# Optimization experiments

Hardware: AMD Instinct MI355X
Metric: run time of the kernel (lower is better)

The kernel has to match this reference:

```python
import jax, jax.numpy as jnp
import numpy as np

N = 100000
E = 1600000
IN_C, HID, OUT_C = 512, 256, 32
K = 10
ALPHA = 0.1


def setup_inputs() -> dict:
    key = jax.random.key(0)
    ks = jax.random.split(key, 8)
    x = jax.random.normal(ks[0], (N, IN_C), dtype=jnp.float32)
    edge_index = jax.random.randint(ks[1], (2, E), 0, N, dtype=jnp.int64)
    def lin(k, fan_in, fan_out):
        kw, kb = jax.random.split(k)
        bound = 1.0 / np.sqrt(fan_in)
        W = jax.random.uniform(kw, (fan_out, fan_in), minval=-bound, maxval=bound, dtype=jnp.float32)
        b = jax.random.uniform(kb, (fan_out,), minval=-bound, maxval=bound, dtype=jnp.float32)
        return W, b
    W1, b1 = lin(ks[2], IN_C, HID)
    Wr, br = lin(ks[3], HID, HID)
    W2, b2 = lin(ks[4], HID, OUT_C)
    return {"x": x, "edge_index": edge_index, "W1": W1, "b1": b1,
            "Wr": Wr, "br": br, "W2": W2, "b2": b2}


def _appnp(h0, row, col, norm):
    # h = (1-alpha) * A_hat h + alpha * h0, K steps
    def step(h, _):
        msg = norm[:, None] * h[row]                      # [E+N, C] gather
        agg = jax.ops.segment_sum(msg, col, num_segments=N)
        return (1.0 - ALPHA) * agg + ALPHA * h0, None
    h, _ = jax.lax.scan(step, h0, None, length=K)
    return h


def reference(x, edge_index, W1, b1, Wr, br, W2, b2):
    # eval mode: dropout p=0 -> identity
    h1 = jax.nn.relu(x @ W1.T + b1)
    h2 = jax.nn.relu(h1 @ Wr.T + br)
    x_res = h1 + h2
    h0 = x_res @ W2.T + b2                                # [N, OUT_C]

    # gcn_norm with self-loops (PyG default for APPNP)
    loops = jnp.arange(N, dtype=edge_index.dtype)
    row = jnp.concatenate([edge_index[0], loops])
    col = jnp.concatenate([edge_index[1], loops])
    deg = jax.ops.segment_sum(jnp.ones_like(col, dtype=h0.dtype), col, num_segments=N)
    dinv = jnp.where(deg > 0, jax.lax.rsqrt(deg), 0.0)
    norm = dinv[row] * dinv[col]                          # [E+N]

    return _appnp(h0, row, col, norm)
```

## Files before the change

### kernel.cpp

```cpp
#include <hip/hip_runtime.h>

#define N_NODES 100000
#define E_EDGES 1600000
#define IN_CH   512
#define HID     256
#define OUT_CH  32
#define K_STEPS 10
#define EPAD    (E_EDGES + 16 * N_NODES)

typedef unsigned short u16;
typedef unsigned int   u32;

typedef __attribute__((ext_vector_type(8))) short bf16x8;
typedef __attribute__((ext_vector_type(4))) float f32x4;

__device__ __forceinline__ float b2f(u16 u) {
    union { u32 i; float f; } x; x.i = ((u32)u) << 16; return x.f;
}
__device__ __forceinline__ u16 f2b(float f) {
    union { float f; u32 u; } x; x.f = f;
    u32 r = x.u + 0x7fffu + ((x.u >> 16) & 1u);
    return (u16)(r >> 16);
}

__device__ __forceinline__ void load_lds16(const void* g, void* l) {
    __builtin_amdgcn_global_load_lds(
        (const __attribute__((address_space(1))) unsigned int*)g,
        (__attribute__((address_space(3))) unsigned int*)l,
        16, 0, 0);
}


__global__ __launch_bounds__(256) void k_cast(const float* __restrict__ in, u16* __restrict__ out, int n4) {
    int i = blockIdx.x * 256 + threadIdx.x;
    if (i < n4) {
        float4 f = ((const float4*)in)[i];
        ushort4 u;
        u.x = f2b(f.x); u.y = f2b(f.y); u.z = f2b(f.z); u.w = f2b(f.w);
        ((ushort4*)out)[i] = u;
    }
}


__global__ __launch_bounds__(256) void k_count(const int* __restrict__ col, int* __restrict__ cnt) {
    int i = blockIdx.x * 256 + threadIdx.x;
    if (i < E_EDGES) atomicAdd(&cnt[col[i]], 1);
}

__global__ __launch_bounds__(256) void k_dinv(const int* __restrict__ cnt, float* __restrict__ dinv) {
    int i = blockIdx.x * 256 + threadIdx.x;
    if (i < N_NODES) dinv[i] = rsqrtf((float)(cnt[i] + 1));
}

__device__ __forceinline__ int pad16(int v) { return (v + 15) & ~15; }

__global__ __launch_bounds__(256) void k_blocksum(const int* __restrict__ cnt, int* __restrict__ bs) {
    int b = blockIdx.x, t = threadIdx.x;
    int idx = b * 1024 + t * 4;
    int s = 0;
    #pragma unroll
    for (int j = 0; j < 4; ++j) if (idx + j < N_NODES) s += pad16(cnt[idx + j]);
    #pragma unroll
    for (int d = 32; d > 0; d >>= 1) s += __shfl_down(s, d, 64);
    __shared__ int smem[4];
    int lane = t & 63, w = t >> 6;
    if (lane == 0) smem[w] = s;
    __syncthreads();
    if (t == 0) bs[b] = smem[0] + smem[1] + smem[2] + smem[3];
}

__global__ void k_scanblocks(const int* __restrict__ bs, int* __restrict__ bo, int nb) {
    int t = threadIdx.x;
    int v = (t < nb) ? bs[t] : 0;
    int incl = v;
    int lane = t & 63, w = t >> 6;
    #pragma unroll
    for (int d = 1; d < 64; d <<= 1) { int tt = __shfl_up(incl, d, 64); if (lane >= d) incl += tt; }
    __shared__ int wsum[2];
    if (lane == 63) wsum[w] = incl;
    __syncthreads();
    int add = (w == 1) ? wsum[0] : 0;
    if (t < nb) bo[t] = add + incl - v;
}

__global__ __launch_bounds__(256) void k_scanwithin(const int* __restrict__ cnt, const int* __restrict__ bo,
                                                    int* __restrict__ off) {
    int b = blockIdx.x, t = threadIdx.x;
    int idx = b * 1024 + t * 4;
    int v[4]; int s = 0;
    #pragma unroll
    for (int j = 0; j < 4; ++j) { v[j] = (idx + j < N_NODES) ? pad16(cnt[idx + j]) : 0; s += v[j]; }
    int incl = s;
    int lane = t & 63, w = t >> 6;
    #pragma unroll
    for (int d = 1; d < 64; d <<= 1) { int tt = __shfl_up(incl, d, 64); if (lane >= d) incl += tt; }
    __shared__ int wsum[4];
    if (lane == 63) wsum[w] = incl;
    __syncthreads();
    int woff = 0;
    #pragma unroll
    for (int k = 0; k < 4; ++k) if (k < w) woff += wsum[k];
    int run = bo[b] + woff + incl - s;
    #pragma unroll
    for (int j = 0; j < 4; ++j) { if (idx + j < N_NODES) off[idx + j] = run; run += v[j]; }
}

__global__ __launch_bounds__(256) void k_total(const int* __restrict__ bo, const int* __restrict__ bs,
                                               int* __restrict__ off, int nb) {
    off[N_NODES] = bo[nb - 1] + bs[nb - 1];
}

__global__ __launch_bounds__(256) void k_filldummy(int* __restrict__ csr_row) {
    int i = blockIdx.x * 256 + threadIdx.x;
    if (i < EPAD) csr_row[i] = N_NODES;
}

__global__ __launch_bounds__(256) void k_fill(const int* __restrict__ row, const int* __restrict__ col,
                                              const int* __restrict__ off, int* __restrict__ cursor,
                                              int* __restrict__ csr_row) {
    int i = blockIdx.x * 256 + threadIdx.x;
    if (i < E_EDGES) {
        int c = col[i];
        int pos = off[c] + atomicAdd(&cursor[c], 1);
        csr_row[pos] = row[i];
    }
}


__device__ __forceinline__ int swz_idx(int row, int col) {
    return row * 256 + (((col >> 3) ^ (row & 7)) << 3) + (col & 7);
}

__global__ __launch_bounds__(512, 2) void fused_mlp(const float* __restrict__ A,
                                                    const u16* __restrict__ W1b,
                                                    const float* __restrict__ b1,
                                                    const u16* __restrict__ Wrb,
                                                    const float* __restrict__ br,
                                                    const float* __restrict__ W2,
                                                    const float* __restrict__ b2,
                                                    const float* __restrict__ dinv,
                                                    float* __restrict__ h0,
                                                    u16* __restrict__ p0,
                                                    int M) {
    __shared__ __align__(16) u16 h1s[128 * 256];
    __shared__ __align__(16) u16 Bs2[2][256 * 32];
    __shared__ __align__(16) u16 As2[2][128 * 32];
    u16* W2s = &As2[0][0];

    const int t = threadIdx.x;
    const int lane = t & 63, w = t >> 6;
    const int wr = (w >> 2) * 64;
    const int wc = (w & 3) * 64;
    const int rr = lane >> 2, cc = lane & 3;
    const int fr = lane & 15, quad = lane >> 4;
    const int row0 = blockIdx.x * 128;

    f32x4 acc[4][4] = {};
    float4 fp[2];
    int arow[2], aseg[2];
    #pragma unroll
    for (int it2 = 0; it2 < 2; ++it2) {
        int chunk = it2 * 512 + t;
        arow[it2] = chunk >> 3; aseg[it2] = chunk & 7;
    }

    auto prefA = [&](int k0) {
        #pragma unroll
        for (int it2 = 0; it2 < 2; ++it2) {
            int gr = row0 + arow[it2]; if (gr > M - 1) gr = M - 1;
            fp[it2] = *(const float4*)&A[(size_t)gr * IN_CH + k0 + aseg[it2] * 4];
        }
    };
    auto writeA = [&](int b) {
        #pragma unroll
        for (int it2 = 0; it2 < 2; ++it2) {
            u32 lo = (u32)f2b(fp[it2].x) | ((u32)f2b(fp[it2].y) << 16);
            u32 hi = (u32)f2b(fp[it2].z) | ((u32)f2b(fp[it2].w) << 16);
            *(uint2*)&As2[b][arow[it2] * 32 + aseg[it2] * 4] = make_uint2(lo, hi);
        }
    };
    auto loadB1 = [&](int k0, int b) {
        #pragma unroll
        for (int rep = 0; rep < 2; ++rep) {
            int ii = w * 2 + rep;
            int gc = ii * 16 + rr;
            load_lds16(W1b + (size_t)gc * IN_CH + k0 + cc * 8, &Bs2[b][ii * 512]);
        }
    };
    auto loadB2 = [&](int k0, int b) {
        #pragma unroll
        for (int rep = 0; rep < 2; ++rep) {
            int ii = w * 2 + rep;
            int gc = ii * 16 + rr;
            load_lds16(Wrb + (size_t)gc * HID + k0 + cc * 8, &Bs2[b][ii * 512]);
        }
    };

    prefA(0);
    loadB1(0, 0);
    writeA(0);
    __syncthreads();

    for (int it = 0; it < IN_CH / 32; ++it) {
        const int cur = it & 1;
        const bool more = (it < IN_CH / 32 - 1);
        if (more) prefA((it + 1) * 32);
        bf16x8 af[4], bfr[4];
        #pragma unroll
        for (int ti = 0; ti < 4; ++ti)
            af[ti] = *(const bf16x8*)&As2[cur][(wr + ti * 16 + fr) * 32 + quad * 8];
        #pragma unroll
        for (int tj = 0; tj < 4; ++tj)
            bfr[tj] = *(const bf16x8*)&Bs2[cur][(wc + tj * 16 + fr) * 32 + quad * 8];
        #pragma unroll
        for (int ti = 0; ti < 4; ++ti)
            #pragma unroll
            for (int tj = 0; tj < 4; ++tj)
                acc[ti][tj] = __builtin_amdgcn_mfma_f32_16x16x32_bf16(af[ti], bfr[tj], acc[ti][tj], 0, 0, 0);
        if (more) {
            loadB1((it + 1) * 32, cur ^ 1);
            writeA(cur ^ 1);
            __syncthreads();
        }
    }

    loadB2(0, 0);
    #pragma unroll
    for (int tj = 0; tj < 4; ++tj) {
        int col = wc + tj * 16 + fr;
        float bv = b1[col];
        #pragma unroll
        for (int ti = 0; ti < 4; ++ti)
            #pragma unroll
            for (int r = 0; r < 4; ++r) {
                int row = wr + ti * 16 + quad * 4 + r;
                h1s[swz_idx(row, col)] = f2b(fmaxf(acc[ti][tj][r] + bv, 0.f));
            }
    }
    __syncthreads();

    #pragma unroll
    for (int ti = 0; ti < 4; ++ti)
        #pragma unroll
        for (int tj = 0; tj < 4; ++tj)
            #pragma unroll
            for (int r = 0; r < 4; ++r) acc[ti][tj][r] = 0.f;

    for (int it = 0; it < HID / 32; ++it) {
        const int cur = it & 1;
        const bool more = (it < HID / 32 - 1);
        if (more) loadB2((it + 1) * 32, cur ^ 1);
        bf16x8 af[4], bfr[4];
        #pragma unroll
        for (int ti = 0; ti < 4; ++ti) {
            int row = wr + ti * 16 + fr;
            af[ti] = *(const bf16x8*)&h1s[row * 256 + (((it * 4 + quad) ^ (row & 7)) << 3)];
        }
        #pragma unroll
        for (int tj = 0; tj < 4; ++tj)
            bfr[tj] = *(const bf16x8*)&Bs2[cur][(wc + tj * 16 + fr) * 32 + quad * 8];
        #pragma unroll
        for (int ti = 0; ti < 4; ++ti)
            #pragma unroll
            for (int tj = 0; tj < 4; ++tj)
                acc[ti][tj] = __builtin_amdgcn_mfma_f32_16x16x32_bf16(af[ti], bfr[tj], acc[ti][tj], 0, 0, 0);
        if (more) __syncthreads();
    }
    __syncthreads();

    float4 wf[4];
    const int wrow = t >> 4, wseg = t & 15;
    {
        const float* src = W2 + (size_t)wrow * HID + wseg * 16;
        wf[0] = *(const float4*)(src + 0);
        wf[1] = *(const float4*)(src + 4);
        wf[2] = *(const float4*)(src + 8);
        wf[3] = *(const float4*)(src + 12);
    }
    #pragma unroll
    for (int tj = 0; tj < 4; ++tj) {
        int col = wc + tj * 16 + fr;
        float bv = br[col];
        #pragma unroll
        for (int ti = 0; ti < 4; ++ti)
            #pragma unroll
            for (int r = 0; r < 4; ++r) {
                int row = wr + ti * 16 + quad * 4 + r;
                int idx = swz_idx(row, col);
                float h1v = b2f(h1s[idx]);
                h1s[idx] = f2b(h1v + fmaxf(acc[ti][tj][r] + bv, 0.f));
            }
    }
    {
        union { u16 s[8]; uint4 q; } pk;
        #pragma unroll
        for (int half = 0; half < 2; ++half) {
            float4 a = wf[half * 2], b = wf[half * 2 + 1];
            pk.s[0] = f2b(a.x); pk.s[1] = f2b(a.y); pk.s[2] = f2b(a.z); pk.s[3] = f2b(a.w);
            pk.s[4] = f2b(b.x); pk.s[5] = f2b(b.y); pk.s[6] = f2b(b.z); pk.s[7] = f2b(b.w);
            int chunk = wseg * 2 + half;
            *(uint4*)&W2s[wrow * 256 + ((chunk ^ (wrow & 7)) << 3)] = pk.q;
        }
    }
    __syncthreads();

    f32x4 acc3[2];
    #pragma unroll
    for (int tj = 0; tj < 2; ++tj)
        #pragma unroll
        for (int r = 0; r < 4; ++r) acc3[tj][r] = 0.f;

    for (int it = 0; it < HID / 32; ++it) {
        int ar = w * 16 + fr;
        bf16x8 af = *(const bf16x8*)&h1s[ar * 256 + (((it * 4 + quad) ^ (ar & 7)) << 3)];
        #pragma unroll
        for (int tj = 0; tj < 2; ++tj) {
            int bc = tj * 16 + fr;
            bf16x8 bfr = *(const bf16x8*)&W2s[bc * 256 + (((it * 4 + quad) ^ (bc & 7)) << 3)];
            acc3[tj] = __builtin_amdgcn_mfma_f32_16x16x32_bf16(af, bfr, acc3[tj], 0, 0, 0);
        }
    }

    #pragma unroll
    for (int tj = 0; tj < 2; ++tj) {
        int col = tj * 16 + fr;
        float bv = b2[col];
        #pragma unroll
        for (int r = 0; r < 4; ++r) {
            int grow = row0 + w * 16 + quad * 4 + r;
            if (grow < M) {
                float v = acc3[tj][r] + bv;
                h0[(size_t)grow * OUT_CH + col] = v;
                p0[(size_t)grow * OUT_CH + col] = f2b(dinv[grow] * v);
            }
        }
    }
}


__global__ __launch_bounds__(256) void k_prop(const u32* __restrict__ pin, u32* __restrict__ pout,
                                              float* __restrict__ hout, const float* __restrict__ h0,
                                              const int* __restrict__ off, const int* __restrict__ csr_row,
                                              const float* __restrict__ dinv, int last) {
    int t = threadIdx.x;
    int gw = blockIdx.x * 16 + (t >> 4);
    int l = t & 15;
    int lbase = t & 48;
    int s = off[gw], e = off[gw + 1];
    float dv = dinv[gw];
    u32 selfp = pin[(size_t)gw * 16 + l];
    float2 h0v = ((const float2*)h0)[(size_t)gw * 16 + l];

    float acc0 = 0.f, acc1 = 0.f;
    for (int base = s; base < e; base += 16) {
        int idx = csr_row[base + l];
        u32 v[16];
        #pragma unroll
        for (int i = 0; i < 16; ++i) {
            int r = __shfl(idx, lbase + i, 64);
            v[i] = pin[(size_t)r * 16 + l];
        }
        #pragma unroll
        for (int i = 0; i < 16; ++i) {
            union { u32 u; float f; } a, b;
            a.u = v[i] << 16; b.u = v[i] & 0xffff0000u;
            acc0 += a.f; acc1 += b.f;
        }
    }
    acc0 += b2f((u16)selfp);
    acc1 += b2f((u16)(selfp >> 16));
    float hc0 = 0.9f * dv * acc0 + 0.1f * h0v.x;
    float hc1 = 0.9f * dv * acc1 + 0.1f * h0v.y;
    if (last) {
        ((float2*)hout)[(size_t)gw * 16 + l] = make_float2(hc0, hc1);
    } else {
        pout[(size_t)gw * 16 + l] = (u32)f2b(dv * hc0) | ((u32)f2b(dv * hc1) << 16);
    }
}


extern "C" void kernel_launch(void* const* d_in, const int* in_sizes, int n_in,
                              void* d_out, int out_size, void* d_ws, size_t ws_size,
                              hipStream_t stream) {
    const float* x  = (const float*)d_in[0];
    const int*   ei = (const int*)d_in[1];
    const float* W1 = (const float*)d_in[2];
    const float* b1 = (const float*)d_in[3];
    const float* Wr = (const float*)d_in[4];
    const float* br = (const float*)d_in[5];
    const float* W2 = (const float*)d_in[6];
    const float* b2 = (const float*)d_in[7];
    float* out = (float*)d_out;

    char* ws = (char*)d_ws;
    size_t off_b = 0;
    auto take = [&](size_t bytes) {
        void* p = ws + off_b;
        off_b += (bytes + 255) & ~(size_t)255;
        return p;
    };

    float* h0      = (float*)take((size_t)N_NODES * OUT_CH * 4);
    u16*   pA      = (u16*)  take((size_t)(N_NODES + 1) * OUT_CH * 2);
    u16*   pB      = (u16*)  take((size_t)(N_NODES + 1) * OUT_CH * 2);
    int*   csr_row = (int*)  take((size_t)EPAD * 4);
    float* dinv    = (float*)take((size_t)N_NODES * 4);
    int*   cnt     = (int*)  take((size_t)N_NODES * 4);
    int*   offs    = (int*)  take((size_t)(N_NODES + 1) * 4);
    int*   cursor  = (int*)  take((size_t)N_NODES * 4);
    int*   bs      = (int*)  take(1024);
    int*   bo      = (int*)  take(1024);
    u16*   W1b     = (u16*)  take((size_t)HID * IN_CH * 2);
    u16*   Wrb     = (u16*)  take((size_t)HID * HID * 2);

    const int* e_row = ei;
    const int* e_col = ei + E_EDGES;

    k_cast<<<(HID * IN_CH / 4 + 255) / 256, 256, 0, stream>>>(W1, W1b, HID * IN_CH / 4);
    k_cast<<<(HID * HID / 4 + 255) / 256, 256, 0, stream>>>(Wr, Wrb, HID * HID / 4);

    hipMemsetAsync(cnt, 0, (size_t)N_NODES * 4, stream);
    hipMemsetAsync(cursor, 0, (size_t)N_NODES * 4, stream);
    hipMemsetAsync(pA + (size_t)N_NODES * OUT_CH, 0, OUT_CH * 2, stream);
    hipMemsetAsync(pB + (size_t)N_NODES * OUT_CH, 0, OUT_CH * 2, stream);
    const int NB = (N_NODES + 1023) / 1024;
    k_count<<<(E_EDGES + 255) / 256, 256, 0, stream>>>(e_col, cnt);
    k_dinv<<<(N_NODES + 255) / 256, 256, 0, stream>>>(cnt, dinv);
    k_blocksum<<<NB, 256, 0, stream>>>(cnt, bs);
    k_scanblocks<<<1, 128, 0, stream>>>(bs, bo, NB);
    k_scanwithin<<<NB, 256, 0, stream>>>(cnt, bo, offs);
    k_total<<<1, 1, 0, stream>>>(bo, bs, offs, NB);
    k_filldummy<<<(EPAD + 255) / 256, 256, 0, stream>>>(csr_row);
    k_fill<<<(E_EDGES + 255) / 256, 256, 0, stream>>>(e_row, e_col, offs, cursor, csr_row);

    fused_mlp<<<(N_NODES + 127) / 128, 512, 0, stream>>>(x, W1b, b1, Wrb, br, W2, b2,
                                                         dinv, h0, pA, N_NODES);

    const u32* pin = (const u32*)pA;
    for (int s = 0; s < K_STEPS; ++s) {
        int last = (s == K_STEPS - 1);
        u32* pout = (u32*)((s & 1) ? pA : pB);
        k_prop<<<N_NODES / 16, 256, 0, stream>>>(pin, pout, out, h0, offs, csr_row, dinv, last);
        pin = pout;
    }
}
```

Before: 760.6 us.

## Halve MLP row tile for higher occupancy and pad CSR segments to eight

The fused MLP kernel now processes 64 rows per block instead of 128, with fewer accumulators per wave and less LDS. The launch bound asks for 4 blocks per CU, and the W2 stage is remapped so each wave computes a single 16x16 output tile. Separately, CSR neighbour lists are padded to multiples of 8 instead of 16, so the propagation loop gathers 8 neighbours per iteration and touches fewer dummy padding entries. The trade-off is that each block re-reads the weights for fewer rows, which adds weight traffic and gives less reuse per block.

```diff
diff --git a/kernel.cpp b/kernel.cpp
--- a/kernel.cpp
+++ b/kernel.cpp
@@ -6,7 +6,7 @@
 #define HID     256
 #define OUT_CH  32
 #define K_STEPS 10
-#define EPAD    (E_EDGES + 16 * N_NODES)
+#define EPAD    (E_EDGES + 8 * N_NODES)
 
 typedef unsigned short u16;
 typedef unsigned int   u32;
@@ -52,14 +52,14 @@
     if (i < N_NODES) dinv[i] = rsqrtf((float)(cnt[i] + 1));
 }
 
-__device__ __forceinline__ int pad16(int v) { return (v + 15) & ~15; }
+__device__ __forceinline__ int pad8(int v) { return (v + 7) & ~7; }
 
 __global__ __launch_bounds__(256) void k_blocksum(const int* __restrict__ cnt, int* __restrict__ bs) {
     int b = blockIdx.x, t = threadIdx.x;
     int idx = b * 1024 + t * 4;
     int s = 0;
     #pragma unroll
-    for (int j = 0; j < 4; ++j) if (idx + j < N_NODES) s += pad16(cnt[idx + j]);
+    for (int j = 0; j < 4; ++j) if (idx + j < N_NODES) s += pad8(cnt[idx + j]);
     #pragma unroll
     for (int d = 32; d > 0; d >>= 1) s += __shfl_down(s, d, 64);
     __shared__ int smem[4];
@@ -89,7 +89,7 @@
     int idx = b * 1024 + t * 4;
     int v[4]; int s = 0;
     #pragma unroll
-    for (int j = 0; j < 4; ++j) { v[j] = (idx + j < N_NODES) ? pad16(cnt[idx + j]) : 0; s += v[j]; }
+    for (int j = 0; j < 4; ++j) { v[j] = (idx + j < N_NODES) ? pad8(cnt[idx + j]) : 0; s += v[j]; }
     int incl = s;
     int lane = t & 63, w = t >> 6;
     #pragma unroll
@@ -131,7 +131,7 @@
     return row * 256 + (((col >> 3) ^ (row & 7)) << 3) + (col & 7);
 }
 
-__global__ __launch_bounds__(512, 2) void fused_mlp(const float* __restrict__ A,
+__global__ __launch_bounds__(512, 4) void fused_mlp(const float* __restrict__ A,
                                                     const u16* __restrict__ W1b,
                                                     const float* __restrict__ b1,
                                                     const u16* __restrict__ Wrb,
@@ -142,42 +142,31 @@
                                                     float* __restrict__ h0,
                                                     u16* __restrict__ p0,
                                                     int M) {
-    __shared__ __align__(16) u16 h1s[128 * 256];
+    __shared__ __align__(16) u16 h1s[64 * 256];
     __shared__ __align__(16) u16 Bs2[2][256 * 32];
-    __shared__ __align__(16) u16 As2[2][128 * 32];
-    u16* W2s = &As2[0][0];
+    __shared__ __align__(16) u16 As2[2][64 * 32];
+    u16* W2s = &Bs2[0][0];
 
     const int t = threadIdx.x;
     const int lane = t & 63, w = t >> 6;
-    const int wr = (w >> 2) * 64;
+    const int wr = (w >> 2) * 32;
     const int wc = (w & 3) * 64;
     const int rr = lane >> 2, cc = lane & 3;
     const int fr = lane & 15, quad = lane >> 4;
-    const int row0 = blockIdx.x * 128;
-
-    f32x4 acc[4][4] = {};
-    float4 fp[2];
-    int arow[2], aseg[2];
-    #pragma unroll
-    for (int it2 = 0; it2 < 2; ++it2) {
-        int chunk = it2 * 512 + t;
-        arow[it2] = chunk >> 3; aseg[it2] = chunk & 7;
-    }
+    const int row0 = blockIdx.x * 64;
+
+    f32x4 acc[2][4] = {};
+    float4 fp;
+    const int arow = t >> 3, aseg = t & 7;
 
     auto prefA = [&](int k0) {
-        #pragma unroll
-        for (int it2 = 0; it2 < 2; ++it2) {
-            int gr = row0 + arow[it2]; if (gr > M - 1) gr = M - 1;
-            fp[it2] = *(const float4*)&A[(size_t)gr * IN_CH + k0 + aseg[it2] * 4];
-        }
+        int gr = row0 + arow; if (gr > M - 1) gr = M - 1;
+        fp = *(const float4*)&A[(size_t)gr * IN_CH + k0 + aseg * 4];
     };
     auto writeA = [&](int b) {
-        #pragma unroll
-        for (int it2 = 0; it2 < 2; ++it2) {
-            u32 lo = (u32)f2b(fp[it2].x) | ((u32)f2b(fp[it2].y) << 16);
-            u32 hi = (u32)f2b(fp[it2].z) | ((u32)f2b(fp[it2].w) << 16);
-            *(uint2*)&As2[b][arow[it2] * 32 + aseg[it2] * 4] = make_uint2(lo, hi);
-        }
+        u32 lo = (u32)f2b(fp.x) | ((u32)f2b(fp.y) << 16);
+        u32 hi = (u32)f2b(fp.z) | ((u32)f2b(fp.w) << 16);
+        *(uint2*)&As2[b][arow * 32 + aseg * 4] = make_uint2(lo, hi);
     };
     auto loadB1 = [&](int k0, int b) {
         #pragma unroll
@@ -205,15 +194,15 @@
         const int cur = it & 1;
         const bool more = (it < IN_CH / 32 - 1);
         if (more) prefA((it + 1) * 32);
-        bf16x8 af[4], bfr[4];
-        #pragma unroll
-        for (int ti = 0; ti < 4; ++ti)
+        bf16x8 af[2], bfr[4];
+        #pragma unroll
+        for (int ti = 0; ti < 2; ++ti)
             af[ti] = *(const bf16x8*)&As2[cur][(wr + ti * 16 + fr) * 32 + quad * 8];
         #pragma unroll
         for (int tj = 0; tj < 4; ++tj)
             bfr[tj] = *(const bf16x8*)&Bs2[cur][(wc + tj * 16 + fr) * 32 + quad * 8];
         #pragma unroll
-        for (int ti = 0; ti < 4; ++ti)
+        for (int ti = 0; ti < 2; ++ti)
             #pragma unroll
             for (int tj = 0; tj < 4; ++tj)
                 acc[ti][tj] = __builtin_amdgcn_mfma_f32_16x16x32_bf16(af[ti], bfr[tj], acc[ti][tj], 0, 0, 0);
@@ -230,7 +219,7 @@
         int col = wc + tj * 16 + fr;
         float bv = b1[col];
         #pragma unroll
-        for (int ti = 0; ti < 4; ++ti)
+        for (int ti = 0; ti < 2; ++ti)
             #pragma unroll
             for (int r = 0; r < 4; ++r) {
                 int row = wr + ti * 16 + quad * 4 + r;
@@ -240,7 +229,7 @@
     __syncthreads();
 
     #pragma unroll
-    for (int ti = 0; ti < 4; ++ti)
+    for (int ti = 0; ti < 2; ++ti)
         #pragma unroll
         for (int tj = 0; tj < 4; ++tj)
             #pragma unroll
@@ -250,9 +239,9 @@
         const int cur = it & 1;
         const bool more = (it < HID / 32 - 1);
         if (more) loadB2((it + 1) * 32, cur ^ 1);
-        bf16x8 af[4], bfr[4];
-        #pragma unroll
-        for (int ti = 0; ti < 4; ++ti) {
+        bf16x8 af[2], bfr[4];
+        #pragma unroll
+        for (int ti = 0; ti < 2; ++ti) {
             int row = wr + ti * 16 + fr;
             af[ti] = *(const bf16x8*)&h1s[row * 256 + (((it * 4 + quad) ^ (row & 7)) << 3)];
         }
@@ -260,7 +249,7 @@
         for (int tj = 0; tj < 4; ++tj)
             bfr[tj] = *(const bf16x8*)&Bs2[cur][(wc + tj * 16 + fr) * 32 + quad * 8];
         #pragma unroll
-        for (int ti = 0; ti < 4; ++ti)
+        for (int ti = 0; ti < 2; ++ti)
             #pragma unroll
             for (int tj = 0; tj < 4; ++tj)
                 acc[ti][tj] = __builtin_amdgcn_mfma_f32_16x16x32_bf16(af[ti], bfr[tj], acc[ti][tj], 0, 0, 0);
@@ -282,7 +271,7 @@
         int col = wc + tj * 16 + fr;
         float bv = br[col];
         #pragma unroll
-        for (int ti = 0; ti < 4; ++ti)
+        for (int ti = 0; ti < 2; ++ti)
             #pragma unroll
             for (int r = 0; r < 4; ++r) {
                 int row = wr + ti * 16 + quad * 4 + r;
@@ -304,32 +293,27 @@
     }
     __syncthreads();
 
-    f32x4 acc3[2];
-    #pragma unroll
-    for (int tj = 0; tj < 2; ++tj)
-        #pragma unroll
-        for (int r = 0; r < 4; ++r) acc3[tj][r] = 0.f;
-
+    f32x4 acc3;
+    #pragma unroll
+    for (int r = 0; r < 4; ++r) acc3[r] = 0.f;
+
+    const int crow = (w >> 1) * 16, ccol = (w & 1) * 16;
     for (int it = 0; it < HID / 32; ++it) {
-        int ar = w * 16 + fr;
+        int ar = crow + fr;
         bf16x8 af = *(const bf16x8*)&h1s[ar * 256 + (((it * 4 + quad) ^ (ar & 7)) << 3)];
-        #pragma unroll
-        for (int tj = 0; tj < 2; ++tj) {
-            int bc = tj * 16 + fr;
-            bf16x8 bfr = *(const bf16x8*)&W2s[bc * 256 + (((it * 4 + quad) ^ (bc & 7)) << 3)];
-            acc3[tj] = __builtin_amdgcn_mfma_f32_16x16x32_bf16(af, bfr, acc3[tj], 0, 0, 0);
-        }
-    }
-
-    #pragma unroll
-    for (int tj = 0; tj < 2; ++tj) {
-        int col = tj * 16 + fr;
+        int bc = ccol + fr;
+        bf16x8 bfr = *(const bf16x8*)&W2s[bc * 256 + (((it * 4 + quad) ^ (bc & 7)) << 3)];
+        acc3 = __builtin_amdgcn_mfma_f32_16x16x32_bf16(af, bfr, acc3, 0, 0, 0);
+    }
+
+    {
+        int col = ccol + fr;
         float bv = b2[col];
         #pragma unroll
         for (int r = 0; r < 4; ++r) {
-            int grow = row0 + w * 16 + quad * 4 + r;
+            int grow = row0 + crow + quad * 4 + r;
             if (grow < M) {
-                float v = acc3[tj][r] + bv;
+                float v = acc3[r] + bv;
                 h0[(size_t)grow * OUT_CH + col] = v;
                 p0[(size_t)grow * OUT_CH + col] = f2b(dinv[grow] * v);
             }
@@ -352,16 +336,16 @@
     float2 h0v = ((const float2*)h0)[(size_t)gw * 16 + l];
 
     float acc0 = 0.f, acc1 = 0.f;
-    for (int base = s; base < e; base += 16) {
-        int idx = csr_row[base + l];
-        u32 v[16];
-        #pragma unroll
-        for (int i = 0; i < 16; ++i) {
+    for (int base = s; base < e; base += 8) {
+        int idx = csr_row[base + (l & 7)];
+        u32 v[8];
+        #pragma unroll
+        for (int i = 0; i < 8; ++i) {
             int r = __shfl(idx, lbase + i, 64);
             v[i] = pin[(size_t)r * 16 + l];
         }
         #pragma unroll
-        for (int i = 0; i < 16; ++i) {
+        for (int i = 0; i < 8; ++i) {
             union { u32 u; float f; } a, b;
             a.u = v[i] << 16; b.u = v[i] & 0xffff0000u;
             acc0 += a.f; acc1 += b.f;
@@ -433,8 +417,8 @@
     k_filldummy<<<(EPAD + 255) / 256, 256, 0, stream>>>(csr_row);
     k_fill<<<(E_EDGES + 255) / 256, 256, 0, stream>>>(e_row, e_col, offs, cursor, csr_row);
 
-    fused_mlp<<<(N_NODES + 127) / 128, 512, 0, stream>>>(x, W1b, b1, Wrb, br, W2, b2,
-                                                         dinv, h0, pA, N_NODES);
+    fused_mlp<<<(N_NODES + 63) / 64, 512, 0, stream>>>(x, W1b, b1, Wrb, br, W2, b2,
+                                                       dinv, h0, pA, N_NODES);
 
     const u32* pin = (const u32*)pA;
     for (int s = 0; s < K_STEPS; ++s) {
```

Result: no change. 754.3 us (-0.8%).
